# Performance work log

Hardware: AMD Instinct MI355X
Metric: run time of the kernel (lower is better)

Reference implementation:

```python
import jax, jax.numpy as jnp
import numpy as np

BETA = 0.2  # 1/5 in the original


def setup_inputs() -> dict:
    key0 = jax.random.key(0)
    kq, kk, kv = jax.random.split(key0, 3)
    B, S, D = 8, 2048, 512
    return {
        "query": jax.random.normal(kq, (B, S, D), dtype=jnp.float32),
        "key": jax.random.normal(kk, (B, S, D), dtype=jnp.float32),
        "value": jax.random.normal(kv, (B, S, D), dtype=jnp.float32),
    }


def reference(query, key, value):
    # NOTE: the original torch module computes W_q/W_k/W_v projections but
    # never uses them; actual scores use the raw inputs. We reproduce the
    # math actually computed.
    B, S, D = query.shape
    # scores: [B, S, S], scaled by sqrt(seq_len) (K = query.shape[1] in torch code)
    scores = jnp.einsum("bsd,btd->bst", query, key) / jnp.sqrt(jnp.float32(S))
    idx = jnp.arange(S)
    dist = jnp.abs(idx[:, None] - idx[None, :]).astype(jnp.float32)
    cauchy_bias = 1.0 / (1.0 + BETA * dist * dist)  # [S, S]
    scores = scores + cauchy_bias
    causal = idx[None, :] > idx[:, None]  # triu with diagonal=1
    scores = jnp.where(causal, -jnp.inf, scores)
    attn = jax.nn.softmax(scores, axis=-1)
    return jnp.einsum("bst,btd->bsd", attn, value)
```

## Files before the change

### kernel.cpp

```cpp
#include <hip/hip_runtime.h>

#define SDIM 2048
#define DDIM 512
#define NB 8

typedef __bf16 bf16x8 __attribute__((ext_vector_type(8)));
typedef float f32x4 __attribute__((ext_vector_type(4)));

__device__ __forceinline__ ushort f2bf(float f) {
  unsigned u = __float_as_uint(f);
  u = (u + 0x7FFFu + ((u >> 16) & 1u)) >> 16;
  return (ushort)u;
}

__global__ void convert_k(const float* __restrict__ K, ushort* __restrict__ Kb) {
  const long N4 = (long)NB * SDIM * DDIM / 4;
  const long stride = (long)gridDim.x * blockDim.x;
  for (long i = (long)blockIdx.x * blockDim.x + threadIdx.x; i < N4; i += stride) {
    float4 k = ((const float4*)K)[i];
    ushort4 o;
    o.x = f2bf(k.x); o.y = f2bf(k.y); o.z = f2bf(k.z); o.w = f2bf(k.w);
    ((ushort4*)Kb)[i] = o;
  }
}

__global__ void transpose_v(const float* __restrict__ V, ushort* __restrict__ Vt) {
  __shared__ float T[64][65];
  int bid = blockIdx.x;
  int b  = bid >> 8;
  int st = (bid >> 3) & 31;
  int dt = bid & 7;
  int t  = threadIdx.x;
  int r  = t >> 4, c4 = (t & 15) << 2;
  const float* src = V + ((size_t)b * SDIM + st * 64) * DDIM + dt * 64;
  #pragma unroll
  for (int i = 0; i < 4; ++i) {
    float4 v = *(const float4*)(src + (size_t)(r + i * 16) * DDIM + c4);
    T[r + i * 16][c4 + 0] = v.x; T[r + i * 16][c4 + 1] = v.y;
    T[r + i * 16][c4 + 2] = v.z; T[r + i * 16][c4 + 3] = v.w;
  }
  __syncthreads();
  ushort* dst = Vt + ((size_t)b * DDIM + dt * 64) * SDIM + st * 64;
  #pragma unroll
  for (int i = 0; i < 4; ++i) {
    int dr = r + i * 16;
    ushort4 o;
    o.x = f2bf(T[c4 + 0][dr]); o.y = f2bf(T[c4 + 1][dr]);
    o.z = f2bf(T[c4 + 2][dr]); o.w = f2bf(T[c4 + 3][dr]);
    *(ushort4*)(dst + (size_t)dr * SDIM + c4) = o;
  }
}

__global__ __launch_bounds__(256, 2) void attn(
    const float* __restrict__ Qf, const ushort* __restrict__ Kb,
    const ushort* __restrict__ Vt, float* __restrict__ out) {
  __shared__ __align__(16) char Ksh[32 * 1024];
  __shared__ __align__(16) char Vsh[32 * 1024];
  __shared__ __align__(16) ushort Psh[32 * 40];
  __shared__ float m_s[2][32], l_s[2][32], pmax_s[2][32], psum_s[2][32];

  const int b  = blockIdx.x & 7;
  const int t  = 63 - (blockIdx.x >> 3);
  const int q0 = t << 5;
  const int tid  = threadIdx.x;
  const int wave = tid >> 6;
  const int lane = tid & 63;
  const int g    = (lane >> 4) & 3;
  const int m16  = lane & 15;
  const int qs   = wave >> 1;
  const int ks   = wave & 1;
  const int dw0  = wave << 7;

  const ushort* kbb = Kb + (size_t)b * SDIM * DDIM;
  const ushort* vtb = Vt + (size_t)b * DDIM * SDIM;

  const float qscale = 0.022097086912079608f;
  bf16x8 qf[16];
  {
    const float* qrow = Qf + ((size_t)b * SDIM + q0 + qs * 16 + m16) * DDIM + g * 8;
    #pragma unroll
    for (int ds = 0; ds < 16; ++ds) {
      float4 u = *(const float4*)(qrow + ds * 32);
      float4 w = *(const float4*)(qrow + ds * 32 + 4);
      union { ushort us[8]; bf16x8 v; } pk;
      pk.us[0] = f2bf(u.x * qscale); pk.us[1] = f2bf(u.y * qscale);
      pk.us[2] = f2bf(u.z * qscale); pk.us[3] = f2bf(u.w * qscale);
      pk.us[4] = f2bf(w.x * qscale); pk.us[5] = f2bf(w.y * qscale);
      pk.us[6] = f2bf(w.z * qscale); pk.us[7] = f2bf(w.w * qscale);
      qf[ds] = pk.v;
    }
  }

  if (tid < 32) { m_s[0][tid] = -1e30f; l_s[0][tid] = 0.0f; }

  const f32x4 zero = {0.f, 0.f, 0.f, 0.f};
  f32x4 acc[2][8];
  #pragma unroll
  for (int qt = 0; qt < 2; ++qt)
    #pragma unroll
    for (int nt = 0; nt < 8; ++nt) acc[qt][nt] = zero;

  const unsigned v_kk = ((lane & 3) ^ ((lane >> 3) & 3)) << 3;

  #pragma unroll
  for (int ji = 0; ji < 8; ++ji) {
    int j = wave * 8 + ji;
    const ushort* src = kbb + (size_t)j * DDIM + ((lane ^ ji) << 3);
    __builtin_amdgcn_global_load_lds((const __attribute__((address_space(1))) void*)src,
        (__attribute__((address_space(3))) void*)(Ksh + j * 1024), 16, 0, 0);
  }

  const int i_row = q0 + qs * 16 + g * 4;
  const int nkt = t + 1;
  for (int kt = 0; kt < nkt; ++kt) {
    const int k0 = kt << 5;
    const int pp = kt & 1;
    __syncthreads();

    #pragma unroll
    for (int vi = 0; vi < 8; ++vi) {
      int v = wave * 8 + vi;
      const ushort* src = vtb + (size_t)(v * 16 + (lane >> 2)) * SDIM + (k0 + v_kk);
      __builtin_amdgcn_global_load_lds((const __attribute__((address_space(1))) void*)src,
          (__attribute__((address_space(3))) void*)(Vsh + v * 1024), 16, 0, 0);
    }

    f32x4 s0 = zero, s1 = zero;
    const char* kptr = Ksh + (ks * 16 + m16) * 1024;
    const unsigned ksw = (unsigned)((m16 & 7) << 4);
    #pragma unroll
    for (int ds = 0; ds < 16; ds += 2) {
      bf16x8 k0f = *(const bf16x8*)(kptr + (((unsigned)(ds * 64 + g * 16)) ^ ksw));
      s0 = __builtin_amdgcn_mfma_f32_16x16x32_bf16(qf[ds], k0f, s0, 0, 0, 0);
      bf16x8 k1f = *(const bf16x8*)(kptr + (((unsigned)((ds + 1) * 64 + g * 16)) ^ ksw));
      s1 = __builtin_amdgcn_mfma_f32_16x16x32_bf16(qf[ds + 1], k1f, s1, 0, 0, 0);
    }

    const int j_col = k0 + ks * 16 + m16;
    const bool diag = (kt == t);
    float sc[4];
    #pragma unroll
    for (int jj = 0; jj < 4; ++jj) {
      float d = (float)(i_row + jj - j_col);
      float bias = __builtin_amdgcn_rcpf(fmaf(0.2f * d, d, 1.0f));
      float s = s0[jj] + s1[jj] + bias;
      if (diag && (j_col > i_row + jj)) s = -1e30f;
      sc[jj] = s;
    }

    float rm[4];
    #pragma unroll
    for (int jj = 0; jj < 4; ++jj) {
      float v = sc[jj];
      v = fmaxf(v, __shfl_xor(v, 1));
      v = fmaxf(v, __shfl_xor(v, 2));
      v = fmaxf(v, __shfl_xor(v, 4));
      v = fmaxf(v, __shfl_xor(v, 8));
      rm[jj] = v;
    }
    if (m16 == 0) {
      #pragma unroll
      for (int jj = 0; jj < 4; ++jj) pmax_s[ks][qs * 16 + g * 4 + jj] = rm[jj];
    }

    __syncthreads();

    if (kt + 1 < nkt) {
      const int k0n = (kt + 1) << 5;
      #pragma unroll
      for (int ji = 0; ji < 8; ++ji) {
        int j = wave * 8 + ji;
        const ushort* src = kbb + (size_t)(k0n + j) * DDIM + ((lane ^ ji) << 3);
        __builtin_amdgcn_global_load_lds((const __attribute__((address_space(1))) void*)src,
            (__attribute__((address_space(3))) void*)(Ksh + j * 1024), 16, 0, 0);
      }
    }

    const int row = lane & 31;
    float mo = m_s[pp][row];
    float tm = fmaxf(pmax_s[0][row], pmax_s[1][row]);
    bool upd = tm > mo + 8.0f;
    float mn = upd ? tm : mo;
    float rr = upd ? __expf(mo - tm) : 1.0f;
    if (wave == 0 && lane < 32) m_s[pp ^ 1][row] = mn;

    float ps[4];
    #pragma unroll
    for (int jj = 0; jj < 4; ++jj) {
      float mq = __shfl(mn, qs * 16 + g * 4 + jj);
      ps[jj] = __expf(sc[jj] - mq);
    }
    #pragma unroll
    for (int jj = 0; jj < 4; ++jj)
      Psh[(qs * 16 + g * 4 + jj) * 40 + ks * 16 + m16] = f2bf(ps[jj]);
    #pragma unroll
    for (int jj = 0; jj < 4; ++jj) {
      float v = ps[jj];
      v += __shfl_xor(v, 1);
      v += __shfl_xor(v, 2);
      v += __shfl_xor(v, 4);
      v += __shfl_xor(v, 8);
      if (m16 == 0) psum_s[ks][qs * 16 + g * 4 + jj] = v;
    }

    if (!__all(rr == 1.0f)) {
      #pragma unroll
      for (int qt = 0; qt < 2; ++qt)
        #pragma unroll
        for (int jj = 0; jj < 4; ++jj) {
          float r2 = __shfl(rr, qt * 16 + g * 4 + jj);
          #pragma unroll
          for (int nt = 0; nt < 8; ++nt) acc[qt][nt][jj] *= r2;
        }
    }

    __syncthreads();

    bf16x8 pa[2];
    #pragma unroll
    for (int qt = 0; qt < 2; ++qt)
      pa[qt] = *(const bf16x8*)((const char*)Psh + (qt * 16 + m16) * 80 + g * 16);
    #pragma unroll
    for (int nt = 0; nt < 8; ++nt) {
      int d = dw0 + nt * 16 + m16;
      bf16x8 vb = *(const bf16x8*)(Vsh + d * 64 + (((unsigned)(g * 16)) ^ (((d >> 1) & 3) << 4)));
      acc[0][nt] = __builtin_amdgcn_mfma_f32_16x16x32_bf16(pa[0], vb, acc[0][nt], 0, 0, 0);
      acc[1][nt] = __builtin_amdgcn_mfma_f32_16x16x32_bf16(pa[1], vb, acc[1][nt], 0, 0, 0);
    }

    if (wave == 0 && lane < 32)
      l_s[pp ^ 1][row] = l_s[pp][row] * rr + psum_s[0][row] + psum_s[1][row];
  }

  __syncthreads();
  const int pf = nkt & 1;
  #pragma unroll
  for (int qt = 0; qt < 2; ++qt) {
    #pragma unroll
    for (int jj = 0; jj < 4; ++jj) {
      float inv = 1.0f / l_s[pf][qt * 16 + g * 4 + jj];
      float* orow = out + ((size_t)b * SDIM + q0 + qt * 16 + g * 4 + jj) * DDIM + dw0 + m16;
      #pragma unroll
      for (int nt = 0; nt < 8; ++nt)
        orow[nt * 16] = acc[qt][nt][jj] * inv;
    }
  }
}

extern "C" void kernel_launch(void* const* d_in, const int* in_sizes, int n_in,
                              void* d_out, int out_size, void* d_ws, size_t ws_size,
                              hipStream_t stream) {
  const float* Q = (const float*)d_in[0];
  const float* K = (const float*)d_in[1];
  const float* V = (const float*)d_in[2];
  float* out = (float*)d_out;
  ushort* Kb = (ushort*)d_ws;
  ushort* Vt = Kb + (size_t)NB * SDIM * DDIM;
  convert_k<<<1024, 256, 0, stream>>>(K, Kb);
  transpose_v<<<2048, 256, 0, stream>>>(V, Vt);
  attn<<<512, 256, 0, stream>>>(Q, Kb, Vt, out);
}
```

Baseline: 317.5 us.

## Load V directly to registers, compute row sums via MFMA, reorder blocks

Removes the V shared-memory staging buffer and loads V fragments from global memory straight into registers at the start of each key tile. Replaces the shuffle-reduced probability sums and l_s bookkeeping with an extra MFMA against a vector of bf16 ones, which accumulates row sums alongside the output. Also replaces __syncthreads with explicit waitcnt+barrier, adds s_setprio around MFMA loops, changes the block-to-tile mapping so the second half of the grid runs short causal tiles first, and doubles the convert_k grid. The intent is to cut LDS traffic and shuffle/sync overhead. The cost is more registers and V reads that are no longer staged through LDS.

```diff
diff --git a/kernel.cpp b/kernel.cpp
--- a/kernel.cpp
+++ b/kernel.cpp
@@ -55,13 +55,14 @@
     const float* __restrict__ Qf, const ushort* __restrict__ Kb,
     const ushort* __restrict__ Vt, float* __restrict__ out) {
   __shared__ __align__(16) char Ksh[32 * 1024];
-  __shared__ __align__(16) char Vsh[32 * 1024];
   __shared__ __align__(16) ushort Psh[32 * 40];
-  __shared__ float m_s[2][32], l_s[2][32], pmax_s[2][32], psum_s[2][32];
-
-  const int b  = blockIdx.x & 7;
-  const int t  = 63 - (blockIdx.x >> 3);
-  const int q0 = t << 5;
+  __shared__ float m_s[2][32], pmax_s[2][32];
+
+  const int bi   = blockIdx.x;
+  const int idx  = bi & 255;
+  const int t    = (bi < 256) ? (63 - (idx >> 3)) : (idx >> 3);
+  const int b    = idx & 7;
+  const int q0   = t << 5;
   const int tid  = threadIdx.x;
   const int wave = tid >> 6;
   const int lane = tid & 63;
@@ -91,16 +92,22 @@
     }
   }
 
-  if (tid < 32) { m_s[0][tid] = -1e30f; l_s[0][tid] = 0.0f; }
+  if (tid < 32) m_s[0][tid] = -1e30f;
+
+  union { ushort us[8]; bf16x8 v; } onesu;
+  #pragma unroll
+  for (int i = 0; i < 8; ++i) onesu.us[i] = 0x3F80;
+  const bf16x8 ones = onesu.v;
 
   const f32x4 zero = {0.f, 0.f, 0.f, 0.f};
   f32x4 acc[2][8];
-  #pragma unroll
-  for (int qt = 0; qt < 2; ++qt)
+  f32x4 acc1[2];
+  #pragma unroll
+  for (int qt = 0; qt < 2; ++qt) {
+    acc1[qt] = zero;
     #pragma unroll
     for (int nt = 0; nt < 8; ++nt) acc[qt][nt] = zero;
-
-  const unsigned v_kk = ((lane & 3) ^ ((lane >> 3) & 3)) << 3;
+  }
 
   #pragma unroll
   for (int ji = 0; ji < 8; ++ji) {
@@ -115,19 +122,18 @@
   for (int kt = 0; kt < nkt; ++kt) {
     const int k0 = kt << 5;
     const int pp = kt & 1;
-    __syncthreads();
-
-    #pragma unroll
-    for (int vi = 0; vi < 8; ++vi) {
-      int v = wave * 8 + vi;
-      const ushort* src = vtb + (size_t)(v * 16 + (lane >> 2)) * SDIM + (k0 + v_kk);
-      __builtin_amdgcn_global_load_lds((const __attribute__((address_space(1))) void*)src,
-          (__attribute__((address_space(3))) void*)(Vsh + v * 1024), 16, 0, 0);
-    }
+    asm volatile("s_waitcnt vmcnt(0) lgkmcnt(0)" ::: "memory");
+    __builtin_amdgcn_s_barrier();
+
+    bf16x8 vb[8];
+    #pragma unroll
+    for (int nt = 0; nt < 8; ++nt)
+      vb[nt] = *(const bf16x8*)(vtb + (size_t)(dw0 + nt * 16 + m16) * SDIM + k0 + g * 8);
 
     f32x4 s0 = zero, s1 = zero;
     const char* kptr = Ksh + (ks * 16 + m16) * 1024;
     const unsigned ksw = (unsigned)((m16 & 7) << 4);
+    __builtin_amdgcn_s_setprio(1);
     #pragma unroll
     for (int ds = 0; ds < 16; ds += 2) {
       bf16x8 k0f = *(const bf16x8*)(kptr + (((unsigned)(ds * 64 + g * 16)) ^ ksw));
@@ -135,6 +141,7 @@
       bf16x8 k1f = *(const bf16x8*)(kptr + (((unsigned)((ds + 1) * 64 + g * 16)) ^ ksw));
       s1 = __builtin_amdgcn_mfma_f32_16x16x32_bf16(qf[ds + 1], k1f, s1, 0, 0, 0);
     }
+    __builtin_amdgcn_s_setprio(0);
 
     const int j_col = k0 + ks * 16 + m16;
     const bool diag = (kt == t);
@@ -148,7 +155,6 @@
       sc[jj] = s;
     }
 
-    float rm[4];
     #pragma unroll
     for (int jj = 0; jj < 4; ++jj) {
       float v = sc[jj];
@@ -156,14 +162,11 @@
       v = fmaxf(v, __shfl_xor(v, 2));
       v = fmaxf(v, __shfl_xor(v, 4));
       v = fmaxf(v, __shfl_xor(v, 8));
-      rm[jj] = v;
-    }
-    if (m16 == 0) {
-      #pragma unroll
-      for (int jj = 0; jj < 4; ++jj) pmax_s[ks][qs * 16 + g * 4 + jj] = rm[jj];
-    }
-
-    __syncthreads();
+      if (m16 == 0) pmax_s[ks][qs * 16 + g * 4 + jj] = v;
+    }
+
+    asm volatile("s_waitcnt lgkmcnt(0)" ::: "memory");
+    __builtin_amdgcn_s_barrier();
 
     if (kt + 1 < nkt) {
       const int k0n = (kt + 1) << 5;
@@ -184,23 +187,11 @@
     float rr = upd ? __expf(mo - tm) : 1.0f;
     if (wave == 0 && lane < 32) m_s[pp ^ 1][row] = mn;
 
-    float ps[4];
     #pragma unroll
     for (int jj = 0; jj < 4; ++jj) {
       float mq = __shfl(mn, qs * 16 + g * 4 + jj);
-      ps[jj] = __expf(sc[jj] - mq);
-    }
-    #pragma unroll
-    for (int jj = 0; jj < 4; ++jj)
-      Psh[(qs * 16 + g * 4 + jj) * 40 + ks * 16 + m16] = f2bf(ps[jj]);
-    #pragma unroll
-    for (int jj = 0; jj < 4; ++jj) {
-      float v = ps[jj];
-      v += __shfl_xor(v, 1);
-      v += __shfl_xor(v, 2);
-      v += __shfl_xor(v, 4);
-      v += __shfl_xor(v, 8);
-      if (m16 == 0) psum_s[ks][qs * 16 + g * 4 + jj] = v;
+      float p = __expf(sc[jj] - mq);
+      Psh[(qs * 16 + g * 4 + jj) * 40 + ks * 16 + m16] = f2bf(p);
     }
 
     if (!__all(rr == 1.0f)) {
@@ -211,34 +202,33 @@
           float r2 = __shfl(rr, qt * 16 + g * 4 + jj);
           #pragma unroll
           for (int nt = 0; nt < 8; ++nt) acc[qt][nt][jj] *= r2;
+          acc1[qt][jj] *= r2;
         }
     }
 
-    __syncthreads();
+    asm volatile("s_waitcnt lgkmcnt(0)" ::: "memory");
+    __builtin_amdgcn_s_barrier();
 
     bf16x8 pa[2];
     #pragma unroll
     for (int qt = 0; qt < 2; ++qt)
       pa[qt] = *(const bf16x8*)((const char*)Psh + (qt * 16 + m16) * 80 + g * 16);
+    __builtin_amdgcn_s_setprio(1);
     #pragma unroll
     for (int nt = 0; nt < 8; ++nt) {
-      int d = dw0 + nt * 16 + m16;
-      bf16x8 vb = *(const bf16x8*)(Vsh + d * 64 + (((unsigned)(g * 16)) ^ (((d >> 1) & 3) << 4)));
-      acc[0][nt] = __builtin_amdgcn_mfma_f32_16x16x32_bf16(pa[0], vb, acc[0][nt], 0, 0, 0);
-      acc[1][nt] = __builtin_amdgcn_mfma_f32_16x16x32_bf16(pa[1], vb, acc[1][nt], 0, 0, 0);
-    }
-
-    if (wave == 0 && lane < 32)
-      l_s[pp ^ 1][row] = l_s[pp][row] * rr + psum_s[0][row] + psum_s[1][row];
-  }
-
-  __syncthreads();
-  const int pf = nkt & 1;
+      acc[0][nt] = __builtin_amdgcn_mfma_f32_16x16x32_bf16(pa[0], vb[nt], acc[0][nt], 0, 0, 0);
+      acc[1][nt] = __builtin_amdgcn_mfma_f32_16x16x32_bf16(pa[1], vb[nt], acc[1][nt], 0, 0, 0);
+    }
+    acc1[0] = __builtin_amdgcn_mfma_f32_16x16x32_bf16(pa[0], ones, acc1[0], 0, 0, 0);
+    acc1[1] = __builtin_amdgcn_mfma_f32_16x16x32_bf16(pa[1], ones, acc1[1], 0, 0, 0);
+    __builtin_amdgcn_s_setprio(0);
+  }
+
   #pragma unroll
   for (int qt = 0; qt < 2; ++qt) {
     #pragma unroll
     for (int jj = 0; jj < 4; ++jj) {
-      float inv = 1.0f / l_s[pf][qt * 16 + g * 4 + jj];
+      float inv = 1.0f / acc1[qt][jj];
       float* orow = out + ((size_t)b * SDIM + q0 + qt * 16 + g * 4 + jj) * DDIM + dw0 + m16;
       #pragma unroll
       for (int nt = 0; nt < 8; ++nt)
@@ -256,7 +246,7 @@
   float* out = (float*)d_out;
   ushort* Kb = (ushort*)d_ws;
   ushort* Vt = Kb + (size_t)NB * SDIM * DDIM;
-  convert_k<<<1024, 256, 0, stream>>>(K, Kb);
+  convert_k<<<2048, 256, 0, stream>>>(K, Kb);
   transpose_v<<<2048, 256, 0, stream>>>(V, Vt);
   attn<<<512, 256, 0, stream>>>(Q, Kb, Vt, out);
 }
```

Result: faster. 283.3 us (-10.8%).
